# Kernel optimization log

Measured on AMD Instinct MI355X. Metric: run time of the kernel, lower is better.

## Reference

```python
import jax, jax.numpy as jnp
import numpy as np

D_HEAD = 64
MASK_FILL = -1000000.0


def setup_inputs() -> dict:
    key = jax.random.key(0)
    ks = jax.random.split(key, 5)
    batch, seq, d_model, n_heads, d_head = 4, 2048, 1024, 16, D_HEAD
    # xavier_uniform bound for [d_model, n_heads, d_head]: treated as fan_in=d_model, fan_out=n_heads*d_head
    bound_qkv = float(np.sqrt(6.0 / (d_model + n_heads * d_head)))
    bound_out = float(np.sqrt(6.0 / (d_head + n_heads * d_model)))
    return {
        "resid": jax.random.normal(ks[0], (batch, seq, d_model), dtype=jnp.float32),
        "W_Q": jax.random.uniform(ks[1], (d_model, n_heads, d_head), jnp.float32, -bound_qkv, bound_qkv),
        "W_K": jax.random.uniform(ks[2], (d_model, n_heads, d_head), jnp.float32, -bound_qkv, bound_qkv),
        "W_V": jax.random.uniform(ks[3], (d_model, n_heads, d_head), jnp.float32, -bound_qkv, bound_qkv),
        "W_out": jax.random.uniform(ks[4], (d_head, n_heads, d_model), jnp.float32, -bound_out, bound_out),
        "b_out": jnp.zeros((d_model,), dtype=jnp.float32),
    }


def reference(resid, W_Q, W_K, W_V, W_out, b_out):
    # resid: [b, s, d]; W_Q/K/V: [d, h, dh]; W_out: [dh, h, d]
    seq = resid.shape[1]
    d_head = W_Q.shape[-1]
    q = jnp.einsum('bsd,dhk->bshk', resid, W_Q)
    k = jnp.einsum('bsd,dhk->bshk', resid, W_K)
    v = jnp.einsum('bsd,dhk->bshk', resid, W_V)
    scores = jnp.einsum('bqhk,bkhd->bhqd', q, k.astype(q.dtype)) if False else jnp.einsum('bqhc,bshc->bhqs', q, k)
    scores = scores / jnp.sqrt(jnp.asarray(d_head, dtype=scores.dtype))
    causal_mask = jnp.triu(jnp.ones((seq, seq), dtype=bool), k=1)
    scores = jnp.where(causal_mask, MASK_FILL, scores)
    probs = jax.nn.softmax(scores, axis=-1)  # [b, h, q, s]
    z = jnp.einsum('bhqs,bshc->bqhc', probs, v)
    out = jnp.einsum('bqhc,chd->bqd', z, W_out) + b_out
    return out
```

## Files before the change

kernel.cpp:

```cpp
#include <hip/hip_runtime.h>
#include <hip/hip_bf16.h>


typedef short s16x8 __attribute__((ext_vector_type(8)));
typedef short s16x4 __attribute__((ext_vector_type(4)));
typedef float f32x4 __attribute__((ext_vector_type(4)));

#define MFMA_BF16(A, B, C) __builtin_amdgcn_mfma_f32_16x16x32_bf16((A), (B), (C), 0, 0, 0)

#if __has_builtin(__builtin_amdgcn_exp2f)
#define EXP2(x) __builtin_amdgcn_exp2f(x)
#else
#define EXP2(x) exp2f(x)
#endif
#if __has_builtin(__builtin_amdgcn_rcpf)
#define RCP(x) __builtin_amdgcn_rcpf(x)
#else
#define RCP(x) (1.0f / (x))
#endif

__device__ __forceinline__ short f2bf(float f) {
    __bf16 h = (__bf16)f;
    return __builtin_bit_cast(short, h);
}

__device__ __forceinline__ void gld16(const unsigned short* g, unsigned short* l) {
    __builtin_amdgcn_global_load_lds(
        (const __attribute__((address_space(1))) unsigned int*)g,
        (__attribute__((address_space(3))) unsigned int*)l, 16, 0, 0);
}

__global__ __launch_bounds__(256) void prep_fused(
    const float* __restrict__ resid, const float* __restrict__ WQ,
    const float* __restrict__ WK, const float* __restrict__ WV,
    const float* __restrict__ Wout,
    unsigned short* __restrict__ residb, unsigned short* __restrict__ Wqkvt,
    unsigned short* __restrict__ W2t)
{
    const int bid = blockIdx.x;
    if (bid < 8192) {
        const int i = bid * 256 + threadIdx.x;
        const float4 v = ((const float4*)resid)[i];
        s16x4 o;
        o[0] = f2bf(v.x); o[1] = f2bf(v.y); o[2] = f2bf(v.z); o[3] = f2bf(v.w);
        *(s16x4*)(residb + (size_t)i * 4) = o;
        return;
    }
    __shared__ unsigned short tile[64][66];
    const int id2 = bid - 8192;
    const int which = id2 >> 8;
    const int sub = id2 & 255;
    const int tx = threadIdx.x & 63, ty = threadIdx.x >> 6;
    if (which < 3) {
        const float* W = which == 0 ? WQ : (which == 1 ? WK : WV);
        unsigned short* Wt = Wqkvt + (size_t)which * 1024 * 1024;
        const int n0 = (sub & 15) * 64, k0 = (sub >> 4) * 64;
        #pragma unroll
        for (int i = ty; i < 64; i += 4)
            tile[i][tx] = (unsigned short)f2bf(W[(size_t)(k0 + i) * 1024 + n0 + tx]);
        __syncthreads();
        #pragma unroll
        for (int i = ty; i < 64; i += 4)
            Wt[(size_t)(n0 + i) * 1024 + k0 + tx] = tile[tx][i];
    } else {
        const int d0 = (sub & 15) * 64, h = sub >> 4;
        #pragma unroll
        for (int c = ty; c < 64; c += 4)
            tile[c][tx] = (unsigned short)f2bf(Wout[(size_t)(c * 16 + h) * 1024 + d0 + tx]);
        __syncthreads();
        #pragma unroll
        for (int i = ty; i < 64; i += 4)
            W2t[(size_t)(d0 + i) * 1024 + h * 64 + tx] = tile[tx][i];
    }
}

template <int MODE>
__global__ __launch_bounds__(512, 2) void gemm_deep(
    const unsigned short* __restrict__ A,
    const unsigned short* __restrict__ Bt,
    unsigned short* __restrict__ Qb, unsigned short* __restrict__ Kb,
    unsigned short* __restrict__ Vt,
    float* __restrict__ Cf, const float* __restrict__ bias)
{
    extern __shared__ __align__(16) unsigned short S[];
    constexpr int LDK = 1024, NT = 16;
    constexpr int NBX = (MODE == 1) ? 12 : 4;
    constexpr int XCH = (MODE == 1) ? 96 : 32;
    const int tid = threadIdx.x, lane = tid & 63, w = tid >> 6;
    const int wm = w >> 2, wn = w & 3;
    const int quad = lane >> 4, fl = lane & 15;

    const int wg  = blockIdx.x;
    const int swz = (wg & 7) * XCH + (wg >> 3);
    const int bx  = swz % NBX, by = swz / NBX;
    const int m0  = by * 128, n0 = bx * 256;

    const int srow = tid >> 2;
    const int sk   = ((tid & 3) ^ ((tid >> 3) & 3)) * 8;
    const unsigned short* pa  = A  + (size_t)(m0 + srow) * LDK + sk;
    const unsigned short* pb0 = Bt + (size_t)(n0 + srow) * LDK + sk;
    const unsigned short* pb1 = Bt + (size_t)(n0 + 128 + srow) * LDK + sk;
    const int dst = tid * 8;

    const int sx   = (quad ^ ((fl >> 1) & 3)) * 8;
    const int arow = (wm * 64 + fl) * 32 + sx;
    const int brow = 8192 + (wn * 64 + fl) * 32 + sx;

    f32x4 acc[4][4];
    #pragma unroll
    for (int m = 0; m < 4; ++m)
        #pragma unroll
        for (int n = 0; n < 4; ++n) acc[m][n] = (f32x4){0.f, 0.f, 0.f, 0.f};

    gld16(pa,       S + dst);
    gld16(pb0,      S + 8192 + dst);
    gld16(pb1,      S + 12288 + dst);
    gld16(pa + 32,  S + 4096 + dst);
    gld16(pb0 + 32, S + 16384 + dst);
    gld16(pb1 + 32, S + 20480 + dst);
    gld16(pa + 64,  S + 24576 + dst);
    gld16(pb0 + 64, S + 24576 + 8192 + dst);
    gld16(pb1 + 64, S + 24576 + 12288 + dst);

    for (int t = 0; t < NT; ++t) {
        unsigned short* Sc = S + (t & 1) * 24576;
        unsigned short* Sn = S + ((t & 1) ^ 1) * 24576;

        if (t < NT - 1) asm volatile("s_waitcnt vmcnt(6)" ::: "memory");
        else            asm volatile("s_waitcnt vmcnt(3)" ::: "memory");
        __builtin_amdgcn_s_barrier();

        s16x8 af[4], bfr[4];
        #pragma unroll
        for (int mi = 0; mi < 4; ++mi) af[mi]  = *(const s16x8*)(Sc + arow + mi * 512);
        #pragma unroll
        for (int ni = 0; ni < 4; ++ni) bfr[ni] = *(const s16x8*)(Sc + brow + ni * 512);
        if (t < NT - 1) {
            const int ka = (t + 1) * 64 + 32;
            gld16(pa + ka,  Sn + 4096 + dst);
            gld16(pb0 + ka, Sn + 16384 + dst);
            gld16(pb1 + ka, Sn + 20480 + dst);
        }
        asm volatile("" ::: "memory");
        __builtin_amdgcn_s_barrier();
        __builtin_amdgcn_s_setprio(1);
        #pragma unroll
        for (int mi = 0; mi < 4; ++mi)
            #pragma unroll
            for (int ni = 0; ni < 4; ++ni)
                acc[mi][ni] = MFMA_BF16(af[mi], bfr[ni], acc[mi][ni]);
        __builtin_amdgcn_s_setprio(0);

        if (t < NT - 1) asm volatile("s_waitcnt vmcnt(6)" ::: "memory");
        else            asm volatile("s_waitcnt vmcnt(0)" ::: "memory");
        __builtin_amdgcn_s_barrier();
        #pragma unroll
        for (int mi = 0; mi < 4; ++mi) af[mi]  = *(const s16x8*)(Sc + 4096 + arow + mi * 512);
        #pragma unroll
        for (int ni = 0; ni < 4; ++ni) bfr[ni] = *(const s16x8*)(Sc + 8192 + brow + ni * 512);
        if (t < NT - 2) {
            const int ka = (t + 2) * 64;
            gld16(pa + ka,  Sc + dst);
            gld16(pb0 + ka, Sc + 8192 + dst);
            gld16(pb1 + ka, Sc + 12288 + dst);
        }
        asm volatile("" ::: "memory");
        __builtin_amdgcn_s_barrier();
        __builtin_amdgcn_s_setprio(1);
        #pragma unroll
        for (int mi = 0; mi < 4; ++mi)
            #pragma unroll
            for (int ni = 0; ni < 4; ++ni)
                acc[mi][ni] = MFMA_BF16(af[mi], bfr[ni], acc[mi][ni]);
        __builtin_amdgcn_s_setprio(0);
    }

    if (MODE == 0) {
        #pragma unroll
        for (int ni = 0; ni < 4; ++ni) {
            const int col = n0 + wn * 64 + ni * 16 + fl;
            const float bv = bias[col];
            #pragma unroll
            for (int mi = 0; mi < 4; ++mi) {
                const int row = m0 + wm * 64 + mi * 16 + quad * 4;
                #pragma unroll
                for (int r = 0; r < 4; ++r)
                    Cf[(size_t)(row + r) * 1024 + col] = acc[mi][ni][r] + bv;
            }
        }
    } else {
        const int which = n0 >> 10;
        if (which < 2) {
            unsigned short* O = which == 0 ? Qb : Kb;
            const int cbase = (n0 & 1023) + wn * 64;
            #pragma unroll
            for (int mi = 0; mi < 4; ++mi) {
                const int row = m0 + wm * 64 + mi * 16 + quad * 4;
                #pragma unroll
                for (int ni = 0; ni < 4; ++ni) {
                    const int col = cbase + ni * 16 + fl;
                    #pragma unroll
                    for (int r = 0; r < 4; ++r)
                        O[(size_t)(row + r) * 1024 + col] = (unsigned short)f2bf(acc[mi][ni][r]);
                }
            }
        } else {
            const int hh = ((n0 - 2048) >> 6) + wn;
            #pragma unroll
            for (int mi = 0; mi < 4; ++mi) {
                const int token = m0 + wm * 64 + mi * 16 + quad * 4;
                const int bb = token >> 11, ss = token & 2047;
                #pragma unroll
                for (int ni = 0; ni < 4; ++ni) {
                    const int cl = ni * 16 + fl;
                    s16x4 pv;
                    pv[0] = f2bf(acc[mi][ni][0]); pv[1] = f2bf(acc[mi][ni][1]);
                    pv[2] = f2bf(acc[mi][ni][2]); pv[3] = f2bf(acc[mi][ni][3]);
                    *(s16x4*)(Vt + (size_t)((bb * 16 + hh) * 64 + cl) * 2048 + ss) = pv;
                }
            }
        }
    }
}

template <bool DIAG>
__device__ __forceinline__ void attn_tile(
    int s0, int wl, int wq0, int fl, int quad,
    const unsigned short* __restrict__ KV, const unsigned short* __restrict__ Vs,
    unsigned short* __restrict__ PbW,
    const s16x8 (&qfr)[2][2], f32x4 (&zt)[2][4], f32x4 (&lsa)[2])
{
    const float SC = 0.18033688011112042f;
    const float M  = 32.0f;
    const s16x8 ones = {16256, 16256, 16256, 16256, 16256, 16256, 16256, 16256};
    #pragma unroll
    for (int c4 = 0; c4 < 4; ++c4) {
        if (DIAG && c4 > wl) break;
        #pragma unroll
        for (int e = 0; e < 2; ++e) {
            const int f = 2 * c4 + e;
            const unsigned short* Krow = KV + (f * 16 + fl) * 72;
            const s16x8 kf0 = *(const s16x8*)(Krow + quad * 8);
            const s16x8 kf1 = *(const s16x8*)(Krow + 32 + quad * 8);
            #pragma unroll
            for (int g = 0; g < 2; ++g) {
                unsigned short* pw = PbW + (g * 16 + fl) * 36 + e * 16 + quad * 4;
                if (DIAG && f > 2 * wl + g) {
                    *(s16x4*)pw = (s16x4){0, 0, 0, 0};
                } else {
                    f32x4 z = (f32x4){0.f, 0.f, 0.f, 0.f};
                    z = MFMA_BF16(kf0, qfr[g][0], z);
                    z = MFMA_BF16(kf1, qfr[g][1], z);
                    float p[4];
                    #pragma unroll
                    for (int r = 0; r < 4; ++r) {
                        float arg = fmaf(z[r], SC, -M);
                        if (DIAG && f == 2 * wl + g) {
                            const int s = s0 + f * 16 + quad * 4 + r;
                            const int qi = wq0 + g * 16 + fl;
                            if (s > qi) arg = -100.f;
                        }
                        p[r] = EXP2(arg);
                    }
                    s16x4 pk;
                    pk[0] = f2bf(p[0]); pk[1] = f2bf(p[1]);
                    pk[2] = f2bf(p[2]); pk[3] = f2bf(p[3]);
                    *(s16x4*)pw = pk;
                }
            }
        }
        const s16x8 pf0 = *(const s16x8*)(PbW + fl * 36 + quad * 8);
        const s16x8 pf1 = *(const s16x8*)(PbW + (16 + fl) * 36 + quad * 8);
        __builtin_amdgcn_s_setprio(1);
        lsa[0] = MFMA_BF16(ones, pf0, lsa[0]);
        lsa[1] = MFMA_BF16(ones, pf1, lsa[1]);
        #pragma unroll
        for (int mf = 0; mf < 4; ++mf) {
            const s16x8 vf = *(const s16x8*)(Vs + (mf * 16 + fl) * 136 + c4 * 32 + quad * 8);
            zt[0][mf] = MFMA_BF16(vf, pf0, zt[0][mf]);
            zt[1][mf] = MFMA_BF16(vf, pf1, zt[1][mf]);
        }
        __builtin_amdgcn_s_setprio(0);
    }
}

__global__ __launch_bounds__(256, 3) void attn_causal(
    const unsigned short* __restrict__ Qb,
    const unsigned short* __restrict__ Kb,
    const unsigned short* __restrict__ Vt,
    unsigned short* __restrict__ Zb)
{
    __shared__ __align__(16) unsigned short KV[17920];
    __shared__ __align__(16) unsigned short Pb[4][32 * 36];
    const int tid = threadIdx.x, lane = tid & 63, w = tid >> 6;
    const int quad = lane >> 4, fl = lane & 15;
    const int lid = blockIdx.x;
    const int qb = 15 - (lid >> 6);
    const int bh = lid & 63, b = bh >> 4, h = bh & 15;
    const int wq0 = qb * 128 + w * 32;
    const int wl = w;

    const unsigned short* Kbase = Kb + (size_t)b * 2048 * 1024 + h * 64;
    const unsigned short* Vbase = Vt + (size_t)bh * 64 * 2048;
    unsigned short* PbW = Pb[w];
    const unsigned short* Vs = KV + 9216;

    s16x8 qfr[2][2];
    #pragma unroll
    for (int g = 0; g < 2; ++g) {
        const unsigned short* Qrow = Qb + (size_t)(b * 2048 + wq0 + g * 16 + fl) * 1024 + h * 64;
        qfr[g][0] = *(const s16x8*)(Qrow + quad * 8);
        qfr[g][1] = *(const s16x8*)(Qrow + 32 + quad * 8);
    }

    const unsigned short* gsp[9];
    int sadv[9];
    unsigned ldsb[9];
    #pragma unroll
    for (int i = 0; i < 9; ++i) {
        const int W = w + 4 * i;
        if (W < 35) {
            const int c = W * 64 + lane;
            if (c < 1152) {
                const int r = c / 9, cl0 = c % 9;
                const int cl = (cl0 == 8) ? 0 : cl0;
                gsp[i] = Kbase + r * 1024 + cl * 8;  sadv[i] = 128 * 1024;
            } else {
                const int cc = c - 1152;
                const int r = cc / 17, cl0 = cc % 17;
                const int cl = (cl0 == 16) ? 0 : cl0;
                gsp[i] = Vbase + r * 2048 + cl * 8;  sadv[i] = 128;
            }
            ldsb[i] = (unsigned)c * 8u;
        }
    }

    f32x4 zt[2][4];
    #pragma unroll
    for (int g = 0; g < 2; ++g)
        #pragma unroll
        for (int mf = 0; mf < 4; ++mf) zt[g][mf] = (f32x4){0.f, 0.f, 0.f, 0.f};
    f32x4 lsa[2] = {(f32x4){0.f, 0.f, 0.f, 0.f}, (f32x4){0.f, 0.f, 0.f, 0.f}};
    const int ntiles = qb + 1;

    for (int kt = 0; kt < ntiles; ++kt) {
        __syncthreads();
        #pragma unroll
        for (int i = 0; i < 9; ++i)
            if (w + 4 * i < 35)
                gld16(gsp[i], KV + ldsb[i]);
        #pragma unroll
        for (int i = 0; i < 9; ++i)
            if (w + 4 * i < 35)
                gsp[i] += sadv[i];
        __syncthreads();

        if (kt < qb) {
            attn_tile<false>(kt << 7, wl, wq0, fl, quad, KV, Vs, PbW, qfr, zt, lsa);
        } else {
            attn_tile<true>(kt << 7, wl, wq0, fl, quad, KV, Vs, PbW, qfr, zt, lsa);
        }
    }
    #pragma unroll
    for (int g = 0; g < 2; ++g) {
        const float inv = RCP(lsa[g][0]);
        unsigned short* Zrow = Zb + (size_t)(b * 2048 + wq0 + g * 16 + fl) * 1024 + h * 64;
        #pragma unroll
        for (int mf = 0; mf < 4; ++mf) {
            s16x4 o;
            o[0] = f2bf(zt[g][mf][0] * inv); o[1] = f2bf(zt[g][mf][1] * inv);
            o[2] = f2bf(zt[g][mf][2] * inv); o[3] = f2bf(zt[g][mf][3] * inv);
            *(s16x4*)(Zrow + mf * 16 + quad * 4) = o;
        }
    }
}

extern "C" void kernel_launch(void* const* d_in, const int* in_sizes, int n_in,
                              void* d_out, int out_size, void* d_ws, size_t ws_size,
                              hipStream_t stream) {
    const float* resid = (const float*)d_in[0];
    const float* WQ    = (const float*)d_in[1];
    const float* WK    = (const float*)d_in[2];
    const float* WV    = (const float*)d_in[3];
    const float* Wout  = (const float*)d_in[4];
    const float* bout  = (const float*)d_in[5];
    float* out = (float*)d_out;

    char* p = (char*)d_ws;
    auto alloc = [&](size_t bytes) { void* r = (void*)p; p += (bytes + 255) & ~(size_t)255; return r; };
    unsigned short* residb = (unsigned short*)alloc(8192ull * 1024 * 2);
    unsigned short* Wqkvt  = (unsigned short*)alloc(3072ull * 1024 * 2);
    unsigned short* W2t    = (unsigned short*)alloc(1024ull * 1024 * 2);
    unsigned short* Qbuf   = (unsigned short*)alloc(8192ull * 1024 * 2);
    unsigned short* Kbuf   = (unsigned short*)alloc(8192ull * 1024 * 2);
    unsigned short* Vtb    = (unsigned short*)alloc(64ull * 64 * 2048 * 2);
    unsigned short* Zbuf   = (unsigned short*)alloc(8192ull * 1024 * 2);

    static bool s_attr = false;
    if (!s_attr) {
        hipFuncSetAttribute(reinterpret_cast<const void*>(gemm_deep<1>),
                            hipFuncAttributeMaxDynamicSharedMemorySize, 98304);
        hipFuncSetAttribute(reinterpret_cast<const void*>(gemm_deep<0>),
                            hipFuncAttributeMaxDynamicSharedMemorySize, 98304);
        s_attr = true;
    }

    prep_fused<<<9216, 256, 0, stream>>>(resid, WQ, WK, WV, Wout, residb, Wqkvt, W2t);
    gemm_deep<1><<<768, 512, 98304, stream>>>(residb, Wqkvt, Qbuf, Kbuf, Vtb,
                                              nullptr, nullptr);
    attn_causal<<<1024, 256, 0, stream>>>(Qbuf, Kbuf, Vtb, Zbuf);
    gemm_deep<0><<<256, 512, 98304, stream>>>(Zbuf, W2t, nullptr, nullptr, nullptr,
                                              out, bout);
}
```

Baseline: 250.2 us.

## Load K/V fragments directly from global memory instead of staging in LDS

Removes the shared-memory K/V staging buffer and the two block barriers per key tile. Each wave now reads its K and V MFMA fragments straight from global memory, relying on L1/L2 to absorb the redundant reads across the four waves. With the large LDS allocation gone, launch bounds are raised to allow more resident blocks. The cost is four times more global/cache traffic for K/V and exposed load latency, since nothing is prefetched.

```diff
diff --git a/kernel.cpp b/kernel.cpp
--- a/kernel.cpp
+++ b/kernel.cpp
@@ -226,7 +226,7 @@
 template <bool DIAG>
 __device__ __forceinline__ void attn_tile(
     int s0, int wl, int wq0, int fl, int quad,
-    const unsigned short* __restrict__ KV, const unsigned short* __restrict__ Vs,
+    const unsigned short* __restrict__ Kt, const unsigned short* __restrict__ Vl,
     unsigned short* __restrict__ PbW,
     const s16x8 (&qfr)[2][2], f32x4 (&zt)[2][4], f32x4 (&lsa)[2])
 {
@@ -239,9 +239,8 @@
         #pragma unroll
         for (int e = 0; e < 2; ++e) {
             const int f = 2 * c4 + e;
-            const unsigned short* Krow = KV + (f * 16 + fl) * 72;
-            const s16x8 kf0 = *(const s16x8*)(Krow + quad * 8);
-            const s16x8 kf1 = *(const s16x8*)(Krow + 32 + quad * 8);
+            const s16x8 kf0 = *(const s16x8*)(Kt + f * 16384);
+            const s16x8 kf1 = *(const s16x8*)(Kt + f * 16384 + 32);
             #pragma unroll
             for (int g = 0; g < 2; ++g) {
                 unsigned short* pw = PbW + (g * 16 + fl) * 36 + e * 16 + quad * 4;
@@ -276,7 +275,7 @@
         lsa[1] = MFMA_BF16(ones, pf1, lsa[1]);
         #pragma unroll
         for (int mf = 0; mf < 4; ++mf) {
-            const s16x8 vf = *(const s16x8*)(Vs + (mf * 16 + fl) * 136 + c4 * 32 + quad * 8);
+            const s16x8 vf = *(const s16x8*)(Vl + mf * 32768 + c4 * 32);
             zt[0][mf] = MFMA_BF16(vf, pf0, zt[0][mf]);
             zt[1][mf] = MFMA_BF16(vf, pf1, zt[1][mf]);
         }
@@ -284,13 +283,12 @@
     }
 }
 
-__global__ __launch_bounds__(256, 3) void attn_causal(
+__global__ __launch_bounds__(256, 5) void attn_causal(
     const unsigned short* __restrict__ Qb,
     const unsigned short* __restrict__ Kb,
     const unsigned short* __restrict__ Vt,
     unsigned short* __restrict__ Zb)
 {
-    __shared__ __align__(16) unsigned short KV[17920];
     __shared__ __align__(16) unsigned short Pb[4][32 * 36];
     const int tid = threadIdx.x, lane = tid & 63, w = tid >> 6;
     const int quad = lane >> 4, fl = lane & 15;
@@ -300,10 +298,7 @@
     const int wq0 = qb * 128 + w * 32;
     const int wl = w;
 
-    const unsigned short* Kbase = Kb + (size_t)b * 2048 * 1024 + h * 64;
-    const unsigned short* Vbase = Vt + (size_t)bh * 64 * 2048;
     unsigned short* PbW = Pb[w];
-    const unsigned short* Vs = KV + 9216;
 
     s16x8 qfr[2][2];
     #pragma unroll
@@ -313,27 +308,10 @@
         qfr[g][1] = *(const s16x8*)(Qrow + 32 + quad * 8);
     }
 
-    const unsigned short* gsp[9];
-    int sadv[9];
-    unsigned ldsb[9];
-    #pragma unroll
-    for (int i = 0; i < 9; ++i) {
-        const int W = w + 4 * i;
-        if (W < 35) {
-            const int c = W * 64 + lane;
-            if (c < 1152) {
-                const int r = c / 9, cl0 = c % 9;
-                const int cl = (cl0 == 8) ? 0 : cl0;
-                gsp[i] = Kbase + r * 1024 + cl * 8;  sadv[i] = 128 * 1024;
-            } else {
-                const int cc = c - 1152;
-                const int r = cc / 17, cl0 = cc % 17;
-                const int cl = (cl0 == 16) ? 0 : cl0;
-                gsp[i] = Vbase + r * 2048 + cl * 8;  sadv[i] = 128;
-            }
-            ldsb[i] = (unsigned)c * 8u;
-        }
-    }
+    const unsigned short* Kt = Kb + (size_t)b * 2048 * 1024 + h * 64
+                                  + (size_t)fl * 1024 + quad * 8;
+    const unsigned short* Vl = Vt + (size_t)bh * 64 * 2048
+                                  + (size_t)fl * 2048 + quad * 8;
 
     f32x4 zt[2][4];
     #pragma unroll
@@ -341,26 +319,14 @@
         #pragma unroll
         for (int mf = 0; mf < 4; ++mf) zt[g][mf] = (f32x4){0.f, 0.f, 0.f, 0.f};
     f32x4 lsa[2] = {(f32x4){0.f, 0.f, 0.f, 0.f}, (f32x4){0.f, 0.f, 0.f, 0.f}};
-    const int ntiles = qb + 1;
-
-    for (int kt = 0; kt < ntiles; ++kt) {
-        __syncthreads();
-        #pragma unroll
-        for (int i = 0; i < 9; ++i)
-            if (w + 4 * i < 35)
-                gld16(gsp[i], KV + ldsb[i]);
-        #pragma unroll
-        for (int i = 0; i < 9; ++i)
-            if (w + 4 * i < 35)
-                gsp[i] += sadv[i];
-        __syncthreads();
-
-        if (kt < qb) {
-            attn_tile<false>(kt << 7, wl, wq0, fl, quad, KV, Vs, PbW, qfr, zt, lsa);
-        } else {
-            attn_tile<true>(kt << 7, wl, wq0, fl, quad, KV, Vs, PbW, qfr, zt, lsa);
-        }
-    }
+
+    for (int kt = 0; kt < qb; ++kt) {
+        attn_tile<false>(kt << 7, wl, wq0, fl, quad, Kt, Vl, PbW, qfr, zt, lsa);
+        Kt += 128 * 1024;
+        Vl += 128;
+    }
+    attn_tile<true>(qb << 7, wl, wq0, fl, quad, Kt, Vl, PbW, qfr, zt, lsa);
+
     #pragma unroll
     for (int g = 0; g < 2; ++g) {
         const float inv = RCP(lsa[g][0]);
```

New measurement: 333.7 us. 33.4% more time.

## Replace LDS P staging with ds_bpermute transposes, raise occupancy, reorder query blocks

Applied to the files above, without the earlier changes.

The per-wave shared-memory buffer for the probability tile is removed. The S-to-P fragment transpose is now done with cross-lane ds_bpermute operations plus selects, which frees LDS and a store/load round trip through shared memory. Launch bounds go from 3 to 4 blocks per CU to use the lower LDS footprint. The query-block ordering is also reshuffled into groups that interleave heavy and light causal tiles for better load balance. The costs are extra bpermute instructions and tighter register pressure from the higher occupancy target.

```diff
diff --git a/kernel.cpp b/kernel.cpp
--- a/kernel.cpp
+++ b/kernel.cpp
@@ -5,6 +5,8 @@
 typedef short s16x8 __attribute__((ext_vector_type(8)));
 typedef short s16x4 __attribute__((ext_vector_type(4)));
 typedef float f32x4 __attribute__((ext_vector_type(4)));
+typedef unsigned u32x2 __attribute__((ext_vector_type(2)));
+typedef unsigned u32x4 __attribute__((ext_vector_type(4)));
 
 #define MFMA_BF16(A, B, C) __builtin_amdgcn_mfma_f32_16x16x32_bf16((A), (B), (C), 0, 0, 0)
 
@@ -225,9 +227,8 @@
 
 template <bool DIAG>
 __device__ __forceinline__ void attn_tile(
-    int s0, int wl, int wq0, int fl, int quad,
+    int s0, int wl, int wq0, int fl, int quad, int a0, int a1,
     const unsigned short* __restrict__ KV, const unsigned short* __restrict__ Vs,
-    unsigned short* __restrict__ PbW,
     const s16x8 (&qfr)[2][2], f32x4 (&zt)[2][4], f32x4 (&lsa)[2])
 {
     const float SC = 0.18033688011112042f;
@@ -236,6 +237,7 @@
     #pragma unroll
     for (int c4 = 0; c4 < 4; ++c4) {
         if (DIAG && c4 > wl) break;
+        u32x2 W[2][2];
         #pragma unroll
         for (int e = 0; e < 2; ++e) {
             const int f = 2 * c4 + e;
@@ -244,9 +246,8 @@
             const s16x8 kf1 = *(const s16x8*)(Krow + 32 + quad * 8);
             #pragma unroll
             for (int g = 0; g < 2; ++g) {
-                unsigned short* pw = PbW + (g * 16 + fl) * 36 + e * 16 + quad * 4;
                 if (DIAG && f > 2 * wl + g) {
-                    *(s16x4*)pw = (s16x4){0, 0, 0, 0};
+                    W[g][e] = (u32x2){0u, 0u};
                 } else {
                     f32x4 z = (f32x4){0.f, 0.f, 0.f, 0.f};
                     z = MFMA_BF16(kf0, qfr[g][0], z);
@@ -265,45 +266,64 @@
                     s16x4 pk;
                     pk[0] = f2bf(p[0]); pk[1] = f2bf(p[1]);
                     pk[2] = f2bf(p[2]); pk[3] = f2bf(p[3]);
-                    *(s16x4*)pw = pk;
+                    W[g][e] = __builtin_bit_cast(u32x2, pk);
                 }
             }
         }
-        const s16x8 pf0 = *(const s16x8*)(PbW + fl * 36 + quad * 8);
-        const s16x8 pf1 = *(const s16x8*)(PbW + (16 + fl) * 36 + quad * 8);
+        s16x8 pf[2];
+        #pragma unroll
+        for (int g = 0; g < 2; ++g) {
+            const int w00 = __builtin_amdgcn_ds_bpermute(a0, (int)W[g][0][0]);
+            const int w10 = __builtin_amdgcn_ds_bpermute(a0, (int)W[g][1][0]);
+            const int w01 = __builtin_amdgcn_ds_bpermute(a0, (int)W[g][0][1]);
+            const int w11 = __builtin_amdgcn_ds_bpermute(a0, (int)W[g][1][1]);
+            const int w02 = __builtin_amdgcn_ds_bpermute(a1, (int)W[g][0][0]);
+            const int w12 = __builtin_amdgcn_ds_bpermute(a1, (int)W[g][1][0]);
+            const int w03 = __builtin_amdgcn_ds_bpermute(a1, (int)W[g][0][1]);
+            const int w13 = __builtin_amdgcn_ds_bpermute(a1, (int)W[g][1][1]);
+            u32x4 pw;
+            pw[0] = (unsigned)(quad < 2 ? w00 : w10);
+            pw[1] = (unsigned)(quad < 2 ? w01 : w11);
+            pw[2] = (unsigned)(quad < 2 ? w02 : w12);
+            pw[3] = (unsigned)(quad < 2 ? w03 : w13);
+            pf[g] = __builtin_bit_cast(s16x8, pw);
+        }
         __builtin_amdgcn_s_setprio(1);
-        lsa[0] = MFMA_BF16(ones, pf0, lsa[0]);
-        lsa[1] = MFMA_BF16(ones, pf1, lsa[1]);
+        lsa[0] = MFMA_BF16(ones, pf[0], lsa[0]);
+        lsa[1] = MFMA_BF16(ones, pf[1], lsa[1]);
         #pragma unroll
         for (int mf = 0; mf < 4; ++mf) {
             const s16x8 vf = *(const s16x8*)(Vs + (mf * 16 + fl) * 136 + c4 * 32 + quad * 8);
-            zt[0][mf] = MFMA_BF16(vf, pf0, zt[0][mf]);
-            zt[1][mf] = MFMA_BF16(vf, pf1, zt[1][mf]);
+            zt[0][mf] = MFMA_BF16(vf, pf[0], zt[0][mf]);
+            zt[1][mf] = MFMA_BF16(vf, pf[1], zt[1][mf]);
         }
         __builtin_amdgcn_s_setprio(0);
     }
 }
 
-__global__ __launch_bounds__(256, 3) void attn_causal(
+__global__ __launch_bounds__(256, 4) void attn_causal(
     const unsigned short* __restrict__ Qb,
     const unsigned short* __restrict__ Kb,
     const unsigned short* __restrict__ Vt,
     unsigned short* __restrict__ Zb)
 {
     __shared__ __align__(16) unsigned short KV[17920];
-    __shared__ __align__(16) unsigned short Pb[4][32 * 36];
     const int tid = threadIdx.x, lane = tid & 63, w = tid >> 6;
     const int quad = lane >> 4, fl = lane & 15;
     const int lid = blockIdx.x;
-    const int qb = 15 - (lid >> 6);
+    const int g8 = lid >> 6;
+    const int q4 = g8 >> 2, qi = g8 & 3;
+    const int qb = q4 == 0 ? 15 - qi : (q4 == 1 ? 8 + qi : (q4 == 2 ? 7 - qi : qi));
     const int bh = lid & 63, b = bh >> 4, h = bh & 15;
     const int wq0 = qb * 128 + w * 32;
     const int wl = w;
 
     const unsigned short* Kbase = Kb + (size_t)b * 2048 * 1024 + h * 64;
     const unsigned short* Vbase = Vt + (size_t)bh * 64 * 2048;
-    unsigned short* PbW = Pb[w];
     const unsigned short* Vs = KV + 9216;
+
+    const int a0 = (fl + 32 * (quad & 1)) << 2;
+    const int a1 = a0 + 64;
 
     s16x8 qfr[2][2];
     #pragma unroll
@@ -356,9 +376,9 @@
         __syncthreads();
 
         if (kt < qb) {
-            attn_tile<false>(kt << 7, wl, wq0, fl, quad, KV, Vs, PbW, qfr, zt, lsa);
+            attn_tile<false>(kt << 7, wl, wq0, fl, quad, a0, a1, KV, Vs, qfr, zt, lsa);
         } else {
-            attn_tile<true>(kt << 7, wl, wq0, fl, quad, KV, Vs, PbW, qfr, zt, lsa);
+            attn_tile<true>(kt << 7, wl, wq0, fl, quad, a0, a1, KV, Vs, qfr, zt, lsa);
         }
     }
     #pragma unroll
```

Result: slower. 343.9 us (+37.4%).
